# Performance work log

Measured on AMD Instinct MI355X. Metric: run time of the kernel, lower is better.

Reference implementation:

```python
import jax, jax.numpy as jnp
import numpy as np

N_NODES = 100000
N_EDGES = 1600000
IN_FEATS = 128
N_HIDDEN = 128
N_CLASSES = 47


def setup_inputs() -> dict:
    key = jax.random.key(0)
    ks = jax.random.split(key, 12)
    def lin(k, fi, fo):
        s = 1.0 / np.sqrt(fi)
        return jax.random.uniform(k, (fi, fo), jnp.float32, -s, s)
    return {
        "x": jax.random.normal(ks[0], (N_NODES, IN_FEATS), jnp.float32),
        "src": jax.random.randint(ks[1], (N_EDGES,), 0, N_NODES, jnp.int32),
        "dst": jax.random.randint(ks[2], (N_EDGES,), 0, N_NODES, jnp.int32),
        "W_self0": lin(ks[3], IN_FEATS, N_HIDDEN),
        "W_neigh0": lin(ks[4], IN_FEATS, N_HIDDEN),
        "b0": jnp.zeros((N_HIDDEN,), jnp.float32),
        "W_self1": lin(ks[5], N_HIDDEN, N_HIDDEN),
        "W_neigh1": lin(ks[6], N_HIDDEN, N_HIDDEN),
        "b1": jnp.zeros((N_HIDDEN,), jnp.float32),
        "W_self2": lin(ks[7], N_HIDDEN, N_CLASSES),
        "W_neigh2": lin(ks[8], N_HIDDEN, N_CLASSES),
        "b2": jnp.zeros((N_CLASSES,), jnp.float32),
    }


def _sage_layer(h, src, dst, W_self, W_neigh, b):
    # DGL SAGEConv 'mean': fc_self(h_dst) + fc_neigh(mean of in-neighbor feats) + bias
    agg = jax.ops.segment_sum(h[src], dst, num_segments=N_NODES)  # [N, d]
    deg = jax.ops.segment_sum(jnp.ones((src.shape[0],), h.dtype), dst,
                              num_segments=N_NODES)
    h_neigh = agg / jnp.maximum(deg, 1.0)[:, None]
    return h @ W_self + h_neigh @ W_neigh + b


def reference(x, src, dst, W_self0, W_neigh0, b0, W_self1, W_neigh1, b1,
              W_self2, W_neigh2, b2):
    h = _sage_layer(x, src, dst, W_self0, W_neigh0, b0)
    h = jax.nn.relu(h)
    h = _sage_layer(h, src, dst, W_self1, W_neigh1, b1)
    h = jax.nn.relu(h)
    h = _sage_layer(h, src, dst, W_self2, W_neigh2, b2)
    return h
```

## Files before the change

### kernel.cpp

```cpp
#include <hip/hip_runtime.h>

#define NN 100000
#define NE 1600000
#define NBK 391
#define CHUNK 8192
#define NBLK ((NE + CHUNK - 1) / CHUNK)
#define MPAD 100096
#define NCAST4 (NN * 32)
#define CASTB 12500
#define GBLK 2048
#define NPW ((NN + 8191) / 8192)

using bf16x8 = __attribute__((ext_vector_type(8))) short;
using f32x4  = __attribute__((ext_vector_type(4))) float;

static __device__ __forceinline__ unsigned short f2bf(float f) {
    unsigned int u = __float_as_uint(f);
    unsigned int r = (u + 0x7FFFu + ((u >> 16) & 1u)) >> 16;
    return (unsigned short)r;
}
static __device__ __forceinline__ float lo16(unsigned int u) {
    return __uint_as_float(u << 16);
}
static __device__ __forceinline__ float hi16(unsigned int u) {
    return __uint_as_float(u & 0xFFFF0000u);
}


__global__ __launch_bounds__(256) void k_hist(const int* __restrict__ dst,
                                              int* __restrict__ ghist) {
    __shared__ int h[NBK];
    int b = blockIdx.x, t = threadIdx.x;
    for (int i = t; i < NBK; i += 256) h[i] = 0;
    __syncthreads();
    int beg = b * CHUNK, end = min(beg + CHUNK, NE);
    for (int i = beg + t; i < end; i += 256)
        atomicAdd(&h[dst[i] >> 8], 1);
    __syncthreads();
    for (int i = t; i < NBK; i += 256) ghist[b * NBK + i] = h[i];
}

__global__ __launch_bounds__(512) void k_basescan(const int* __restrict__ ghist,
                                                  int* __restrict__ boff,
                                                  int* __restrict__ gbase) {
    __shared__ int s[512];
    int t = threadIdx.x;
    int tot = 0;
    if (t < NBK)
        for (int blk = 0; blk < NBLK; ++blk) tot += ghist[blk * NBK + t];
    s[t] = tot;
    __syncthreads();
    for (int o = 1; o < 512; o <<= 1) {
        int u = (t >= o) ? s[t - o] : 0;
        __syncthreads();
        s[t] += u;
        __syncthreads();
    }
    int base = s[t] - tot;
    if (t <= NBK) boff[t] = base;
    if (t < NBK) {
        int run = base;
        for (int blk = 0; blk < NBLK; ++blk) {
            int g = ghist[blk * NBK + t];
            gbase[blk * NBK + t] = run;
            run += g;
        }
    }
}

__global__ __launch_bounds__(256) void k_scatter(const int* __restrict__ src,
                                                 const int* __restrict__ dst,
                                                 const int* __restrict__ gbase,
                                                 unsigned int* __restrict__ eb) {
    __shared__ int cur[NBK];
    int b = blockIdx.x, t = threadIdx.x;
    for (int i = t; i < NBK; i += 256) cur[i] = gbase[b * NBK + i];
    __syncthreads();
    int beg = b * CHUNK, end = min(beg + CHUNK, NE);
    for (int i = beg + t; i < end; i += 256) {
        int d = dst[i];
        int p = atomicAdd(&cur[d >> 8], 1);
        eb[p] = ((unsigned int)(d & 255) << 24) | (unsigned int)src[i];
    }
}

__global__ __launch_bounds__(256) void k_csr(const unsigned int* __restrict__ eb,
                                             const int* __restrict__ boff,
                                             int* __restrict__ rp,
                                             int* __restrict__ col) {
    __shared__ int h[256];
    __shared__ int sc[256];
    __shared__ int cur[256];
    int b = blockIdx.x, t = threadIdx.x;
    h[t] = 0;
    __syncthreads();
    int beg = boff[b], end = boff[b + 1];
    for (int e = beg + t; e < end; e += 256)
        atomicAdd(&h[eb[e] >> 24], 1);
    __syncthreads();
    int c = h[t];
    sc[t] = c;
    __syncthreads();
    for (int o = 1; o < 256; o <<= 1) {
        int v = (t >= o) ? sc[t - o] : 0;
        __syncthreads();
        sc[t] += v;
        __syncthreads();
    }
    int excl = beg + sc[t] - c;
    int node = (b << 8) + t;
    if (node < NN) rp[node] = excl;
    if (node == NN - 1) rp[NN] = NE;
    cur[t] = excl;
    __syncthreads();
    for (int e = beg + t; e < end; e += 256) {
        unsigned int p = eb[e];
        int pos = atomicAdd(&cur[p >> 24], 1);
        col[pos] = (int)(p & 0xFFFFFFu);
    }
}


__global__ __launch_bounds__(256) void k_prep(
        const float4* __restrict__ x4, ushort4* __restrict__ XB4,
        const float* __restrict__ Ws0, const float* __restrict__ Wn0,
        unsigned short* __restrict__ BT0,
        const float* __restrict__ Ws1, const float* __restrict__ Wn1,
        unsigned short* __restrict__ BT1,
        const float* __restrict__ Ws2, const float* __restrict__ Wn2,
        unsigned short* __restrict__ BT2) {
    int bid = blockIdx.x, t = threadIdx.x;
    if (bid < CASTB) {
        int i = bid * 256 + t;
        float4 v = x4[i];
        ushort4 o;
        o.x = f2bf(v.x); o.y = f2bf(v.y); o.z = f2bf(v.z); o.w = f2bf(v.w);
        XB4[i] = o;
    } else if (bid < CASTB + 128) {
        int idx = (bid - CASTB) * 256 + t;
        int k = idx >> 7, n = idx & 127;
        float v = (k < 128) ? Ws0[k * 128 + n] : Wn0[(k - 128) * 128 + n];
        BT0[n * 256 + k] = f2bf(v);
    } else if (bid < CASTB + 256) {
        int idx = (bid - CASTB - 128) * 256 + t;
        int k = idx >> 7, n = idx & 127;
        float v = (k < 128) ? Ws1[k * 128 + n] : Wn1[(k - 128) * 128 + n];
        BT1[n * 256 + k] = f2bf(v);
    } else {
        int idx = (bid - CASTB - 256) * 256 + t;
        if (idx < 96 * 128) {
            int n = idx >> 7, k = idx & 127;
            float v = 0.f;
            if (n < 48) { if (n < 47) v = Ws2[k * 47 + n]; }
            else        { int cc = n - 48; if (cc < 47) v = Wn2[k * 47 + cc]; }
            BT2[n * 128 + k] = f2bf(v);
        }
    }
}


__global__ __launch_bounds__(256) void k_gather128(
        const uint2* __restrict__ hb2,
        const int* __restrict__ rp, const int* __restrict__ col,
        uint2* __restrict__ hnb2) {
    int wave = blockIdx.x * 4 + (threadIdx.x >> 6);
    int lane = threadIdx.x & 63;
    int half = lane >> 5, l32 = lane & 31;
    int n0 = wave * NPW;
    int n1 = min(n0 + NPW, NN);
    for (int node = n0; node < n1; ++node) {
        int beg = rp[node], end = rp[node + 1];
        float a0 = 0.f, a1 = 0.f, a2 = 0.f, a3 = 0.f;
        float b0 = 0.f, b1 = 0.f, b2 = 0.f, b3 = 0.f;
        int e = beg;
        for (; e + 8 <= end; e += 8) {
            int c0 = col[e + half];
            int c1 = col[e + 2 + half];
            int c2 = col[e + 4 + half];
            int c3 = col[e + 6 + half];
            uint2 v0 = hb2[(size_t)c0 * 32 + l32];
            uint2 v1 = hb2[(size_t)c1 * 32 + l32];
            uint2 v2 = hb2[(size_t)c2 * 32 + l32];
            uint2 v3 = hb2[(size_t)c3 * 32 + l32];
            a0 += lo16(v0.x); a1 += hi16(v0.x); a2 += lo16(v0.y); a3 += hi16(v0.y);
            b0 += lo16(v1.x); b1 += hi16(v1.x); b2 += lo16(v1.y); b3 += hi16(v1.y);
            a0 += lo16(v2.x); a1 += hi16(v2.x); a2 += lo16(v2.y); a3 += hi16(v2.y);
            b0 += lo16(v3.x); b1 += hi16(v3.x); b2 += lo16(v3.y); b3 += hi16(v3.y);
        }
        for (; e < end; e += 2) {
            if (e + half < end) {
                uint2 v = hb2[(size_t)col[e + half] * 32 + l32];
                a0 += lo16(v.x); a1 += hi16(v.x); a2 += lo16(v.y); a3 += hi16(v.y);
            }
        }
        float s0 = a0 + b0, s1 = a1 + b1, s2 = a2 + b2, s3 = a3 + b3;
        s0 += __shfl_xor(s0, 32);
        s1 += __shfl_xor(s1, 32);
        s2 += __shfl_xor(s2, 32);
        s3 += __shfl_xor(s3, 32);
        if (half == 0) {
            float d = (float)(end - beg);
            float inv = (d > 0.f) ? 1.0f / d : 0.0f;
            uint2 o;
            o.x = ((unsigned int)f2bf(s1 * inv) << 16) | (unsigned int)f2bf(s0 * inv);
            o.y = ((unsigned int)f2bf(s3 * inv) << 16) | (unsigned int)f2bf(s2 * inv);
            hnb2[(size_t)node * 32 + l32] = o;
        }
    }
}


__global__ __launch_bounds__(256, 2) void k_mgemm(
        const unsigned short* __restrict__ A0,
        const unsigned short* __restrict__ A1,
        const unsigned short* __restrict__ BT,
        const float* __restrict__ bias,
        unsigned short* __restrict__ outB) {
    int t = threadIdx.x;
    int lane = t & 63, wid = t >> 6;
    int wm = wid >> 1, wn = wid & 1;
    int lr = lane & 15, lg = lane >> 4;
    int row0 = blockIdx.x * 128 + wm * 64;
    int colw = wn * 64;
    f32x4 zero = {0.f, 0.f, 0.f, 0.f};
    f32x4 acc[4][4];
#pragma unroll
    for (int a = 0; a < 4; ++a)
#pragma unroll
        for (int b = 0; b < 4; ++b) acc[a][b] = zero;

#pragma unroll
    for (int p = 0; p < 2; ++p) {
        const unsigned short* A = p ? A1 : A0;
        bf16x8 bReg[4][4];
#pragma unroll
        for (int nf = 0; nf < 4; ++nf)
#pragma unroll
            for (int ks = 0; ks < 4; ++ks)
                bReg[nf][ks] = *(const bf16x8*)&BT[(size_t)(colw + nf * 16 + lr) * 256 + p * 128 + ks * 32 + lg * 8];
#pragma unroll
        for (int mf = 0; mf < 4; ++mf) {
            const unsigned short* Ar = A + (size_t)(row0 + mf * 16 + lr) * 128;
            bf16x8 aReg[4];
#pragma unroll
            for (int ks = 0; ks < 4; ++ks)
                aReg[ks] = *(const bf16x8*)&Ar[ks * 32 + lg * 8];
#pragma unroll
            for (int ks = 0; ks < 4; ++ks)
#pragma unroll
                for (int nf = 0; nf < 4; ++nf)
                    acc[mf][nf] = __builtin_amdgcn_mfma_f32_16x16x32_bf16(
                        aReg[ks], bReg[nf][ks], acc[mf][nf], 0, 0, 0);
        }
    }
    __syncthreads();
#pragma unroll
    for (int nf = 0; nf < 4; ++nf) {
        int cidx = colw + nf * 16 + lr;
        float bb = bias[cidx];
#pragma unroll
        for (int mf = 0; mf < 4; ++mf) {
#pragma unroll
            for (int j = 0; j < 4; ++j) {
                int row = row0 + mf * 16 + lg * 4 + j;
                if (row < NN) {
                    float v = fmaxf(acc[mf][nf][j] + bb, 0.f);
                    outB[(size_t)row * 128 + cidx] = f2bf(v);
                }
            }
        }
    }
}


__global__ __launch_bounds__(256, 2) void k_mgemm47(
        const unsigned short* __restrict__ A,
        const unsigned short* __restrict__ BT2,
        const float* __restrict__ bias,
        float* __restrict__ S,
        unsigned short* __restrict__ TB) {
    int t = threadIdx.x;
    int lane = t & 63, wid = t >> 6;
    int wm = wid >> 1, wn = wid & 1;
    int lr = lane & 15, lg = lane >> 4;
    int row0 = blockIdx.x * 128 + wm * 64;
    int colw = wn * 48;
    f32x4 zero = {0.f, 0.f, 0.f, 0.f};
    f32x4 acc[4][3];
#pragma unroll
    for (int a = 0; a < 4; ++a)
#pragma unroll
        for (int b = 0; b < 3; ++b) acc[a][b] = zero;

    bf16x8 bReg[3][4];
#pragma unroll
    for (int nf = 0; nf < 3; ++nf)
#pragma unroll
        for (int ks = 0; ks < 4; ++ks)
            bReg[nf][ks] = *(const bf16x8*)&BT2[(size_t)(colw + nf * 16 + lr) * 128 + ks * 32 + lg * 8];
#pragma unroll
    for (int mf = 0; mf < 4; ++mf) {
        const unsigned short* Ar = A + (size_t)(row0 + mf * 16 + lr) * 128;
        bf16x8 aReg[4];
#pragma unroll
        for (int ks = 0; ks < 4; ++ks)
            aReg[ks] = *(const bf16x8*)&Ar[ks * 32 + lg * 8];
#pragma unroll
        for (int ks = 0; ks < 4; ++ks)
#pragma unroll
            for (int nf = 0; nf < 3; ++nf)
                acc[mf][nf] = __builtin_amdgcn_mfma_f32_16x16x32_bf16(
                    aReg[ks], bReg[nf][ks], acc[mf][nf], 0, 0, 0);
    }
#pragma unroll
    for (int nf = 0; nf < 3; ++nf) {
        int cidx = colw + nf * 16 + lr;
#pragma unroll
        for (int mf = 0; mf < 4; ++mf) {
#pragma unroll
            for (int j = 0; j < 4; ++j) {
                int row = row0 + mf * 16 + lg * 4 + j;
                if (row < NN) {
                    float v = acc[mf][nf][j];
                    if (cidx < 47)
                        S[(size_t)row * 48 + cidx] = v + bias[cidx];
                    else if (cidx >= 48)
                        TB[(size_t)row * 48 + (cidx - 48)] = f2bf(v);
                }
            }
        }
    }
}


__global__ __launch_bounds__(256) void k_gather47(
        const unsigned int* __restrict__ TB32,
        const float2* __restrict__ S2,
        const int* __restrict__ rp, const int* __restrict__ col,
        float* __restrict__ out) {
    int wave = blockIdx.x * 4 + (threadIdx.x >> 6);
    int lane = threadIdx.x & 63;
    int half = lane >> 5, l32 = lane & 31;
    bool act = l32 < 24;
    int n0 = wave * NPW;
    int n1 = min(n0 + NPW, NN);
    for (int node = n0; node < n1; ++node) {
        int beg = rp[node], end = rp[node + 1];
        float c0a = 0.f, c1a = 0.f, c0b = 0.f, c1b = 0.f;
        int e = beg;
        for (; e + 8 <= end; e += 8) {
            int i0 = col[e + half];
            int i1 = col[e + 2 + half];
            int i2 = col[e + 4 + half];
            int i3 = col[e + 6 + half];
            if (act) {
                unsigned int u0 = TB32[(size_t)i0 * 24 + l32];
                unsigned int u1 = TB32[(size_t)i1 * 24 + l32];
                unsigned int u2 = TB32[(size_t)i2 * 24 + l32];
                unsigned int u3 = TB32[(size_t)i3 * 24 + l32];
                c0a += lo16(u0); c1a += hi16(u0);
                c0b += lo16(u1); c1b += hi16(u1);
                c0a += lo16(u2); c1a += hi16(u2);
                c0b += lo16(u3); c1b += hi16(u3);
            }
        }
        for (; e < end; e += 2) {
            if (act && e + half < end) {
                unsigned int u = TB32[(size_t)col[e + half] * 24 + l32];
                c0a += lo16(u); c1a += hi16(u);
            }
        }
        float s0 = c0a + c0b, s1 = c1a + c1b;
        s0 += __shfl_xor(s0, 32);
        s1 += __shfl_xor(s1, 32);
        if (half == 0 && act) {
            float d = (float)(end - beg);
            float inv = (d > 0.f) ? 1.0f / d : 0.0f;
            float2 sv = S2[(size_t)node * 24 + l32];
            int c = l32 * 2;
            out[(size_t)node * 47 + c] = sv.x + s0 * inv;
            if (c + 1 < 47) out[(size_t)node * 47 + c + 1] = sv.y + s1 * inv;
        }
    }
}


static inline size_t align_up(size_t x, size_t a) { return (x + a - 1) / a * a; }

extern "C" void kernel_launch(void* const* d_in, const int* in_sizes, int n_in,
                              void* d_out, int out_size, void* d_ws, size_t ws_size,
                              hipStream_t stream) {
    const float* x   = (const float*)d_in[0];
    const int* src   = (const int*)d_in[1];
    const int* dst   = (const int*)d_in[2];
    const float* Ws0 = (const float*)d_in[3];
    const float* Wn0 = (const float*)d_in[4];
    const float* b0  = (const float*)d_in[5];
    const float* Ws1 = (const float*)d_in[6];
    const float* Wn1 = (const float*)d_in[7];
    const float* b1  = (const float*)d_in[8];
    const float* Ws2 = (const float*)d_in[9];
    const float* Wn2 = (const float*)d_in[10];
    const float* b2  = (const float*)d_in[11];
    float* out = (float*)d_out;

    char* ws = (char*)d_ws;
    size_t off = 0;
    auto alloc = [&](size_t bytes) -> void* {
        void* p = ws + off; off = align_up(off + bytes, 256); return p;
    };
    int* row_ptr = (int*)alloc((size_t)(NN + 1) * 4);
    int* boff    = (int*)alloc((size_t)(NBK + 1) * 4);
    int* gbase   = (int*)alloc((size_t)NBLK * NBK * 4);
    int* ghist   = (int*)alloc((size_t)NBLK * NBK * 4);
    int* col     = (int*)alloc((size_t)NE * 4);
    unsigned short* XB  = (unsigned short*)alloc((size_t)MPAD * 128 * 2);
    unsigned short* BT0 = (unsigned short*)alloc(128 * 256 * 2);
    unsigned short* BT1 = (unsigned short*)alloc(128 * 256 * 2);
    unsigned short* BT2 = (unsigned short*)alloc(96 * 128 * 2);
    char* big = (char*)alloc((size_t)NN * 48 * 4 * 2);
    unsigned int* eb    = (unsigned int*)big;
    unsigned int* HNB   = (unsigned int*)big;
    float* S            = (float*)big;
    unsigned short* TB  = (unsigned short*)(big + (size_t)NN * 48 * 4);

    k_hist<<<NBLK, 256, 0, stream>>>(dst, ghist);
    k_basescan<<<1, 512, 0, stream>>>(ghist, boff, gbase);
    k_scatter<<<NBLK, 256, 0, stream>>>(src, dst, gbase, eb);
    k_csr<<<NBK, 256, 0, stream>>>(eb, boff, row_ptr, col);

    k_prep<<<CASTB + 256 + 48, 256, 0, stream>>>(
        (const float4*)x, (ushort4*)XB, Ws0, Wn0, BT0, Ws1, Wn1, BT1, Ws2, Wn2, BT2);

    int mgrid = MPAD / 128;

    k_gather128<<<GBLK, 256, 0, stream>>>((const uint2*)XB, row_ptr, col, (uint2*)HNB);
    k_mgemm<<<mgrid, 256, 0, stream>>>(XB, (const unsigned short*)HNB, BT0, b0, XB);
    k_gather128<<<GBLK, 256, 0, stream>>>((const uint2*)XB, row_ptr, col, (uint2*)HNB);
    k_mgemm<<<mgrid, 256, 0, stream>>>(XB, (const unsigned short*)HNB, BT1, b1, XB);
    k_mgemm47<<<mgrid, 256, 0, stream>>>(XB, BT2, b2, S, TB);
    k_gather47<<<GBLK, 256, 0, stream>>>((const unsigned int*)TB, (const float2*)S,
                                         row_ptr, col, out);
}
```

Measured before the change: 363.4 us.

## Fuse neighbor mean-gather into layer GEMM via swizzled LDS tile

The separate gather and GEMM kernels for the two hidden layers become one kernel. Each block gathers neighbor means for its 128 rows into an XOR-swizzled shared-memory tile, then runs the MFMA GEMM reading the neighbor operand from LDS. This removes the HNB round trip through global memory and one launch per layer. Ping-pong XB buffers are added because the fused kernel reads arbitrary neighbor rows while writing its output. The trade-offs are 32KB of LDS per block, which lowers occupancy for the latency-bound gather, coarser work distribution (782 blocks of 128 nodes), and a fully predicated 16-edge unroll.

```diff
diff --git a/kernel.cpp b/kernel.cpp
--- a/kernel.cpp
+++ b/kernel.cpp
@@ -159,39 +159,48 @@
 }
 
 
-__global__ __launch_bounds__(256) void k_gather128(
-        const uint2* __restrict__ hb2,
+__global__ __launch_bounds__(256, 2) void k_fused(
+        const unsigned short* __restrict__ Ain,
+        const unsigned short* __restrict__ BT,
+        const float* __restrict__ bias,
         const int* __restrict__ rp, const int* __restrict__ col,
-        uint2* __restrict__ hnb2) {
-    int wave = blockIdx.x * 4 + (threadIdx.x >> 6);
-    int lane = threadIdx.x & 63;
+        unsigned short* __restrict__ outB) {
+    __shared__ char hnl[128 * 256];
+    int t = threadIdx.x;
+    int lane = t & 63, wid = t >> 6;
+    int row0 = blockIdx.x * 128;
     int half = lane >> 5, l32 = lane & 31;
-    int n0 = wave * NPW;
-    int n1 = min(n0 + NPW, NN);
-    for (int node = n0; node < n1; ++node) {
-        int beg = rp[node], end = rp[node + 1];
+    const uint2* hb2 = (const uint2*)Ain;
+
+    for (int i = 0; i < 32; ++i) {
+        int lrow = wid * 32 + i;
+        int node = row0 + lrow;
+        int beg = 0, end = 0;
+        if (node < NN) { beg = rp[node]; end = rp[node + 1]; }
         float a0 = 0.f, a1 = 0.f, a2 = 0.f, a3 = 0.f;
         float b0 = 0.f, b1 = 0.f, b2 = 0.f, b3 = 0.f;
-        int e = beg;
-        for (; e + 8 <= end; e += 8) {
-            int c0 = col[e + half];
-            int c1 = col[e + 2 + half];
-            int c2 = col[e + 4 + half];
-            int c3 = col[e + 6 + half];
-            uint2 v0 = hb2[(size_t)c0 * 32 + l32];
-            uint2 v1 = hb2[(size_t)c1 * 32 + l32];
-            uint2 v2 = hb2[(size_t)c2 * 32 + l32];
-            uint2 v3 = hb2[(size_t)c3 * 32 + l32];
+        for (int e = beg; e < end; e += 16) {
+            int o0 = e + half,      o1 = e + 2 + half,  o2 = e + 4 + half,  o3 = e + 6 + half;
+            int o4 = e + 8 + half,  o5 = e + 10 + half, o6 = e + 12 + half, o7 = e + 14 + half;
+            bool p0 = o0 < end, p1 = o1 < end, p2 = o2 < end, p3 = o3 < end;
+            bool p4 = o4 < end, p5 = o5 < end, p6 = o6 < end, p7 = o7 < end;
+            uint2 z = make_uint2(0u, 0u);
+            uint2 v0 = p0 ? hb2[(size_t)col[o0] * 32 + l32] : z;
+            uint2 v1 = p1 ? hb2[(size_t)col[o1] * 32 + l32] : z;
+            uint2 v2 = p2 ? hb2[(size_t)col[o2] * 32 + l32] : z;
+            uint2 v3 = p3 ? hb2[(size_t)col[o3] * 32 + l32] : z;
+            uint2 v4 = p4 ? hb2[(size_t)col[o4] * 32 + l32] : z;
+            uint2 v5 = p5 ? hb2[(size_t)col[o5] * 32 + l32] : z;
+            uint2 v6 = p6 ? hb2[(size_t)col[o6] * 32 + l32] : z;
+            uint2 v7 = p7 ? hb2[(size_t)col[o7] * 32 + l32] : z;
             a0 += lo16(v0.x); a1 += hi16(v0.x); a2 += lo16(v0.y); a3 += hi16(v0.y);
             b0 += lo16(v1.x); b1 += hi16(v1.x); b2 += lo16(v1.y); b3 += hi16(v1.y);
             a0 += lo16(v2.x); a1 += hi16(v2.x); a2 += lo16(v2.y); a3 += hi16(v2.y);
             b0 += lo16(v3.x); b1 += hi16(v3.x); b2 += lo16(v3.y); b3 += hi16(v3.y);
-        }
-        for (; e < end; e += 2) {
-            if (e + half < end) {
-                uint2 v = hb2[(size_t)col[e + half] * 32 + l32];
-                a0 += lo16(v.x); a1 += hi16(v.x); a2 += lo16(v.y); a3 += hi16(v.y);
-            }
+            a0 += lo16(v4.x); a1 += hi16(v4.x); a2 += lo16(v4.y); a3 += hi16(v4.y);
+            b0 += lo16(v5.x); b1 += hi16(v5.x); b2 += lo16(v5.y); b3 += hi16(v5.y);
+            a0 += lo16(v6.x); a1 += hi16(v6.x); a2 += lo16(v6.y); a3 += hi16(v6.y);
+            b0 += lo16(v7.x); b1 += hi16(v7.x); b2 += lo16(v7.y); b3 += hi16(v7.y);
         }
         float s0 = a0 + b0, s1 = a1 + b1, s2 = a2 + b2, s3 = a3 + b3;
         s0 += __shfl_xor(s0, 32);
@@ -204,23 +213,15 @@
             uint2 o;
             o.x = ((unsigned int)f2bf(s1 * inv) << 16) | (unsigned int)f2bf(s0 * inv);
             o.y = ((unsigned int)f2bf(s3 * inv) << 16) | (unsigned int)f2bf(s2 * inv);
-            hnb2[(size_t)node * 32 + l32] = o;
-        }
-    }
-}
-
-
-__global__ __launch_bounds__(256, 2) void k_mgemm(
-        const unsigned short* __restrict__ A0,
-        const unsigned short* __restrict__ A1,
-        const unsigned short* __restrict__ BT,
-        const float* __restrict__ bias,
-        unsigned short* __restrict__ outB) {
-    int t = threadIdx.x;
-    int lane = t & 63, wid = t >> 6;
+            int bco = (l32 * 8) ^ ((lrow & 7) << 4);
+            *(uint2*)&hnl[lrow * 256 + bco] = o;
+        }
+    }
+    __syncthreads();
+
     int wm = wid >> 1, wn = wid & 1;
     int lr = lane & 15, lg = lane >> 4;
-    int row0 = blockIdx.x * 128 + wm * 64;
+    int rw0 = row0 + wm * 64;
     int colw = wn * 64;
     f32x4 zero = {0.f, 0.f, 0.f, 0.f};
     f32x4 acc[4][4];
@@ -229,18 +230,16 @@
 #pragma unroll
         for (int b = 0; b < 4; ++b) acc[a][b] = zero;
 
-#pragma unroll
-    for (int p = 0; p < 2; ++p) {
-        const unsigned short* A = p ? A1 : A0;
+    {
         bf16x8 bReg[4][4];
 #pragma unroll
         for (int nf = 0; nf < 4; ++nf)
 #pragma unroll
             for (int ks = 0; ks < 4; ++ks)
-                bReg[nf][ks] = *(const bf16x8*)&BT[(size_t)(colw + nf * 16 + lr) * 256 + p * 128 + ks * 32 + lg * 8];
+                bReg[nf][ks] = *(const bf16x8*)&BT[(size_t)(colw + nf * 16 + lr) * 256 + ks * 32 + lg * 8];
 #pragma unroll
         for (int mf = 0; mf < 4; ++mf) {
-            const unsigned short* Ar = A + (size_t)(row0 + mf * 16 + lr) * 128;
+            const unsigned short* Ar = Ain + (size_t)(rw0 + mf * 16 + lr) * 128;
             bf16x8 aReg[4];
 #pragma unroll
             for (int ks = 0; ks < 4; ++ks)
@@ -253,7 +252,30 @@
                         aReg[ks], bReg[nf][ks], acc[mf][nf], 0, 0, 0);
         }
     }
-    __syncthreads();
+    {
+        bf16x8 bReg[4][4];
+#pragma unroll
+        for (int nf = 0; nf < 4; ++nf)
+#pragma unroll
+            for (int ks = 0; ks < 4; ++ks)
+                bReg[nf][ks] = *(const bf16x8*)&BT[(size_t)(colw + nf * 16 + lr) * 256 + 128 + ks * 32 + lg * 8];
+#pragma unroll
+        for (int mf = 0; mf < 4; ++mf) {
+            int ar = wm * 64 + mf * 16 + lr;
+            bf16x8 aReg[4];
+#pragma unroll
+            for (int ks = 0; ks < 4; ++ks) {
+                int bco = (ks * 64 + lg * 16) ^ ((ar & 7) << 4);
+                aReg[ks] = *(const bf16x8*)&hnl[ar * 256 + bco];
+            }
+#pragma unroll
+            for (int ks = 0; ks < 4; ++ks)
+#pragma unroll
+                for (int nf = 0; nf < 4; ++nf)
+                    acc[mf][nf] = __builtin_amdgcn_mfma_f32_16x16x32_bf16(
+                        aReg[ks], bReg[nf][ks], acc[mf][nf], 0, 0, 0);
+        }
+    }
 #pragma unroll
     for (int nf = 0; nf < 4; ++nf) {
         int cidx = colw + nf * 16 + lr;
@@ -262,7 +284,7 @@
         for (int mf = 0; mf < 4; ++mf) {
 #pragma unroll
             for (int j = 0; j < 4; ++j) {
-                int row = row0 + mf * 16 + lg * 4 + j;
+                int row = rw0 + mf * 16 + lg * 4 + j;
                 if (row < NN) {
                     float v = fmaxf(acc[mf][nf][j] + bb, 0.f);
                     outB[(size_t)row * 128 + cidx] = f2bf(v);
@@ -414,13 +436,13 @@
     int* gbase   = (int*)alloc((size_t)NBLK * NBK * 4);
     int* ghist   = (int*)alloc((size_t)NBLK * NBK * 4);
     int* col     = (int*)alloc((size_t)NE * 4);
-    unsigned short* XB  = (unsigned short*)alloc((size_t)MPAD * 128 * 2);
+    unsigned short* XB0 = (unsigned short*)alloc((size_t)MPAD * 128 * 2);
+    unsigned short* XB1 = (unsigned short*)alloc((size_t)MPAD * 128 * 2);
     unsigned short* BT0 = (unsigned short*)alloc(128 * 256 * 2);
     unsigned short* BT1 = (unsigned short*)alloc(128 * 256 * 2);
     unsigned short* BT2 = (unsigned short*)alloc(96 * 128 * 2);
-    char* big = (char*)alloc((size_t)NN * 48 * 4 * 2);
-    unsigned int* eb    = (unsigned int*)big;
-    unsigned int* HNB   = (unsigned int*)big;
+    char* big = (char*)alloc((size_t)NN * 48 * 4 + (size_t)NN * 48 * 2);
+    unsigned int* eb    = (unsigned int*)XB1;
     float* S            = (float*)big;
     unsigned short* TB  = (unsigned short*)(big + (size_t)NN * 48 * 4);
 
@@ -430,15 +452,13 @@
     k_csr<<<NBK, 256, 0, stream>>>(eb, boff, row_ptr, col);
 
     k_prep<<<CASTB + 256 + 48, 256, 0, stream>>>(
-        (const float4*)x, (ushort4*)XB, Ws0, Wn0, BT0, Ws1, Wn1, BT1, Ws2, Wn2, BT2);
+        (const float4*)x, (ushort4*)XB0, Ws0, Wn0, BT0, Ws1, Wn1, BT1, Ws2, Wn2, BT2);
 
     int mgrid = MPAD / 128;
 
-    k_gather128<<<GBLK, 256, 0, stream>>>((const uint2*)XB, row_ptr, col, (uint2*)HNB);
-    k_mgemm<<<mgrid, 256, 0, stream>>>(XB, (const unsigned short*)HNB, BT0, b0, XB);
-    k_gather128<<<GBLK, 256, 0, stream>>>((const uint2*)XB, row_ptr, col, (uint2*)HNB);
-    k_mgemm<<<mgrid, 256, 0, stream>>>(XB, (const unsigned short*)HNB, BT1, b1, XB);
-    k_mgemm47<<<mgrid, 256, 0, stream>>>(XB, BT2, b2, S, TB);
+    k_fused<<<mgrid, 256, 0, stream>>>(XB0, BT0, b0, row_ptr, col, XB1);
+    k_fused<<<mgrid, 256, 0, stream>>>(XB1, BT1, b1, row_ptr, col, XB0);
+    k_mgemm47<<<mgrid, 256, 0, stream>>>(XB0, BT2, b2, S, TB);
     k_gather47<<<GBLK, 256, 0, stream>>>((const unsigned int*)TB, (const float2*)S,
                                          row_ptr, col, out);
 }
```

Result: slower. 504.7 us (+38.9%).
